# Kernel tuning notes

Measured on AMD Instinct MI355X. Metric: run time of the kernel, lower is better.

The kernel has to match this reference:

```python
import jax, jax.numpy as jnp
import numpy as np

T, B = 2048, 256
NX, NY, NU, ND = 128, 64, 32, 16


def setup_inputs() -> dict:
    key = jax.random.key(0)
    ks = jax.random.split(key, 12)
    # weights scaled to keep the closed-loop recursion numerically stable
    return {
        "Yp": jax.random.normal(ks[0], (T, B, NY), jnp.float32),
        "Up": jax.random.normal(ks[1], (T, B, NU), jnp.float32),
        "Dp": jax.random.normal(ks[2], (T, B, ND), jnp.float32),
        "Wfx": jax.random.normal(ks[3], (NX, NX), jnp.float32) * (0.9 / np.sqrt(NX)),
        "bfx": jax.random.normal(ks[4], (NX,), jnp.float32) * 0.01,
        "Wfu": jax.random.normal(ks[5], (NU, NX), jnp.float32) * (1.0 / np.sqrt(NU)),
        "bfu": jax.random.normal(ks[6], (NX,), jnp.float32) * 0.01,
        "Wfd": jax.random.normal(ks[7], (ND, NX), jnp.float32) * (1.0 / np.sqrt(ND)),
        "bfd": jax.random.normal(ks[8], (NX,), jnp.float32) * 0.01,
        "Wfy": jax.random.normal(ks[9], (NX, NY), jnp.float32) * (1.0 / np.sqrt(NX)),
        "bfy": jax.random.normal(ks[10], (NY,), jnp.float32) * 0.01,
        # constant (non-trainable) filter buffers, matching the torch module
        "Q": jnp.eye(NX, dtype=jnp.float32),
        "R": jnp.eye(NY, dtype=jnp.float32),
        "P0": jnp.eye(NX, dtype=jnp.float32),
        "L0": jnp.zeros((NX, NY), jnp.float32),
        "x0": jnp.zeros((1, NX), jnp.float32),
    }


def reference(Yp, Up, Dp, Wfx, bfx, Wfu, bfu, Wfd, bfd, Wfy, bfy, Q, R, P0, L0, x0):
    nx = Wfx.shape[0]
    Bsz = Yp.shape[1]
    eye = jnp.eye(nx, dtype=Yp.dtype)
    # x0 is zeros(1, nx); broadcast to batch so scan carry has fixed shape
    x_init = jnp.broadcast_to(x0, (Bsz, nx))

    def step(carry, inp):
        x, P, L = carry
        ym, u, d = inp  # [B,ny], [B,nu], [B,nd]
        # prediction (slim linear: x @ W + b)
        x = x @ Wfx + bfx + u @ Wfu + bfu + d @ Wfd + bfd
        y = x @ Wfy + bfy
        P = Wfx @ (P @ Wfx.T) + Q
        # correction with previous gain L (as in the torch code)
        x = x + (ym - y) @ L.T
        S = R + Wfy.T @ (P @ Wfy)              # [ny,ny]
        L = (P @ Wfy) @ jnp.linalg.inv(S)      # [nx,ny]
        P = eye - L @ (Wfy.T @ P)              # faithful to source (I - L H P)
        return (x, P, L), None

    (x, P, L), _ = jax.lax.scan(step, (x_init, P0, L0), (Yp, Up, Dp))
    return x  # 'x0' output of the estimator
```

## Files before the change

kernel.cpp:

```cpp
#include <hip/hip_runtime.h>

#define T_STEPS 2048
#define BATCH   256
#define NXX     128
#define NYY     64
#define NUU     32
#define NDD     16

#define CCH     64
#define NCH     (T_STEPS / CCH)

#define SWZ(i, j) (((i) << 6) + ((j) ^ ((i) & 31)))

__device__ __forceinline__ float4 ld4swz(const float* s, int row, int cg) {
  return *(const float4*)(s + (row << 6) + (cg ^ (row & 28)));
}
__device__ __forceinline__ void st4swz(float* s, int row, int cg, const float4& v) {
  *(float4*)(s + (row << 6) + (cg ^ (row & 28))) = v;
}

__global__ __launch_bounds__(256, 1)
void lkf_gains(const float* __restrict__ F, const float* __restrict__ W,
               const float* __restrict__ Q, const float* __restrict__ R,
               const float* __restrict__ P0, float* __restrict__ Linf,
               float* __restrict__ LinfT, float* __restrict__ CWq,
               float* __restrict__ tmpA, float* __restrict__ tmpB)
{
  __shared__ __align__(16) float sG[NXX * NYY];
  __shared__ __align__(16) float sS[NYY * NYY];
  __shared__ __align__(16) float sM[NYY * NYY];
  __shared__ __align__(16) float sW[NXX * NYY];
  float* sCol = sM;
  float* sRed = sM;
  const int tid = threadIdx.x;

  for (int idx = tid; idx < NXX * NYY; idx += 256)
    sW[SWZ(idx >> 6, idx & 63)] = W[idx];
  for (int idx = tid; idx < NXX * NYY; idx += 256) {
    const int k = idx >> 6, j = idx & 63;
    float acc = 0.f;
    for (int i = 0; i < NXX; ++i) acc += F[i * NXX + k] * W[i * NYY + j];
    tmpA[idx] = acc;
  }
  __syncthreads();
  for (int idx = tid; idx < NXX * NYY; idx += 256) {
    const int i = idx >> 6, j = idx & 63;
    float acc = 0.f;
    for (int k = 0; k < NXX; ++k) acc += F[i * NXX + k] * tmpA[k * NYY + j];
    for (int k = 0; k < NXX; ++k) acc += Q[i * NXX + k] * W[k * NYY + j];
    CWq[idx] = acc;
  }
  for (int idx = tid; idx < NXX * NXX; idx += 256) {
    const int i = idx >> 7, j = idx & 127;
    float acc = 0.f;
    for (int k = 0; k < NXX; ++k) acc += P0[i * NXX + k] * F[j * NXX + k];
    tmpB[idx] = acc;
  }
  __syncthreads();
  for (int idx = tid; idx < NXX * NXX; idx += 256) {
    const int i = idx >> 7, j = idx & 127;
    float acc = Q[idx];
    for (int k = 0; k < NXX; ++k) acc += F[i * NXX + k] * tmpB[k * NXX + j];
    tmpA[idx] = acc;
  }
  __syncthreads();
  for (int idx = tid; idx < NXX * NYY; idx += 256) {
    const int i = idx >> 6, j = idx & 63;
    float acc = 0.f;
    for (int k = 0; k < NXX; ++k) acc += tmpA[i * NXX + k] * W[k * NYY + j];
    sG[SWZ(i, j)] = acc;
  }
  __syncthreads();
  for (int idx = tid; idx < NXX * NXX; idx += 256)
    tmpB[idx] = F[(idx & 127) * NXX + (idx >> 7)];
  const float* Ft = tmpB;

  const int i16 = (tid >> 4) * 4;
  const int j16 = (tid & 15) * 4;
  const int i32 = (tid >> 3) * 4;
  const int j32 = (tid & 7) * 8;

  float cwq[4][8], rreg[4][4];
#pragma unroll
  for (int a = 0; a < 4; ++a)
#pragma unroll
    for (int b = 0; b < 8; ++b)
      cwq[a][b] = CWq[(i32 + a) * NYY + j32 + b];
#pragma unroll
  for (int a = 0; a < 4; ++a)
#pragma unroll
    for (int b = 0; b < 4; ++b)
      rreg[a][b] = R[(i16 + a) * NYY + j16 + b];

  float prevG[4][8], diff[4][8];
#pragma unroll
  for (int a = 0; a < 4; ++a)
#pragma unroll
    for (int b = 0; b < 8; ++b) { prevG[a][b] = 1e30f; diff[a][b] = 0.f; }
  int   cc = 0;
  bool  fin = false;
  float prevDelta = 1e30f;
  __syncthreads();

  for (int t = 0; t < T_STEPS; ++t) {
    {
      float acc[4][4];
#pragma unroll
      for (int a = 0; a < 4; ++a)
#pragma unroll
        for (int b = 0; b < 4; ++b) acc[a][b] = 0.f;
      for (int kb = 0; kb < NXX; kb += 4) {
#pragma unroll
        for (int kk = 0; kk < 4; ++kk) {
          const int k = kb + kk;
          const float4 wv = ld4swz(sW, k, i16);
          const float4 gv = ld4swz(sG, k, j16);
          const float* wf = (const float*)&wv;
          const float* gf = (const float*)&gv;
#pragma unroll
          for (int a = 0; a < 4; ++a)
#pragma unroll
            for (int b = 0; b < 4; ++b)
              acc[a][b] += wf[a ^ kk] * gf[b ^ kk];
        }
      }
#pragma unroll
      for (int a = 0; a < 4; ++a) {
        float4 w; float* wf = (float*)&w;
#pragma unroll
        for (int b = 0; b < 4; ++b) wf[b ^ a] = rreg[a][b] + acc[a][b];
        st4swz(sS, i16 + a, j16, w);
      }
    }
    __syncthreads();

    for (int kb = 0; kb < NYY; kb += 4) {
#pragma unroll
      for (int kk = 0; kk < 4; ++kk) {
        const int k = kb + kk;
        if (tid < NYY) {
          const int j = tid;
          const float piv  = sS[SWZ(k, k)];
          const float pinv = 1.0f / piv;
          const float cv   = sS[SWZ(j, k)];
          sCol[j] = cv;
          if (j != k) {
            sS[SWZ(k, j)] *= pinv;
            sS[SWZ(j, k)] = 0.f;
          } else {
            sS[SWZ(k, k)] = pinv;
          }
        }
        __syncthreads();
        {
          const float4 rk = ld4swz(sS, k, j16);
          const float4 cf = *(const float4*)(sCol + i16);
          const float* rkf = (const float*)&rk;
          const float* cff = (const float*)&cf;
#pragma unroll
          for (int a = 0; a < 4; ++a) {
            if (i16 + a != k) {
              float4 ri = ld4swz(sS, i16 + a, j16);
              float* rif = (float*)&ri;
              const float f = cff[a];
#pragma unroll
              for (int b = 0; b < 4; ++b)
                rif[b ^ a] -= f * rkf[b ^ kk];
              st4swz(sS, i16 + a, j16, ri);
            }
          }
        }
        __syncthreads();
      }
    }

    if (fin || t == T_STEPS - 1) {
      float acc[4][8];
#pragma unroll
      for (int a = 0; a < 4; ++a)
#pragma unroll
        for (int b = 0; b < 8; ++b) acc[a][b] = 0.f;
      for (int k = 0; k < NYY; ++k) {
        float g4[4], s8[8];
#pragma unroll
        for (int a = 0; a < 4; ++a) g4[a] = sG[SWZ(i32 + a, k)];
#pragma unroll
        for (int b = 0; b < 8; ++b) s8[b] = sS[SWZ(k, j32 + b)];
#pragma unroll
        for (int a = 0; a < 4; ++a)
#pragma unroll
          for (int b = 0; b < 8; ++b) acc[a][b] += g4[a] * s8[b];
      }
#pragma unroll
      for (int a = 0; a < 4; ++a)
#pragma unroll
        for (int b = 0; b < 8; ++b) {
          Linf[(i32 + a) * NYY + j32 + b]  = acc[a][b];
          LinfT[(j32 + b) * NXX + i32 + a] = acc[a][b];
        }
      break;
    }

    {
      float acc[4][8];
#pragma unroll
      for (int a = 0; a < 4; ++a)
#pragma unroll
        for (int b = 0; b < 8; ++b) acc[a][b] = 0.f;
      for (int kb = 0; kb < NXX; kb += 4) {
#pragma unroll
        for (int kk = 0; kk < 4; ++kk) {
          const int k = kb + kk;
          const float4 fv  = *(const float4*)(Ft + k * NXX + i32);
          const float4 gv0 = ld4swz(sG, k, j32);
          const float4 gv1 = ld4swz(sG, k, j32 + 4);
          const float* ff  = (const float*)&fv;
          const float* gf0 = (const float*)&gv0;
          const float* gf1 = (const float*)&gv1;
#pragma unroll
          for (int a = 0; a < 4; ++a)
#pragma unroll
            for (int b = 0; b < 4; ++b) {
              acc[a][b]     += ff[a] * gf0[b ^ kk];
              acc[a][b + 4] += ff[a] * gf1[b ^ kk];
            }
        }
      }
      __syncthreads();
#pragma unroll
      for (int a = 0; a < 4; ++a) {
        float4 w0, w1; float* wf0 = (float*)&w0; float* wf1 = (float*)&w1;
#pragma unroll
        for (int b = 0; b < 4; ++b) {
          wf0[b ^ a] = acc[a][b];
          wf1[b ^ a] = acc[a][b + 4];
        }
        st4swz(sG, i32 + a, j32, w0);
        st4swz(sG, i32 + a, j32 + 4, w1);
      }
    }
    __syncthreads();

    {
      float acc[4][4];
#pragma unroll
      for (int a = 0; a < 4; ++a)
#pragma unroll
        for (int b = 0; b < 4; ++b) acc[a][b] = 0.f;
      for (int kb = 0; kb < NXX; kb += 4) {
#pragma unroll
        for (int kk = 0; kk < 4; ++kk) {
          const int k = kb + kk;
          const float4 hv = ld4swz(sG, k, i16);
          const float4 wv = ld4swz(sW, k, j16);
          const float* hf = (const float*)&hv;
          const float* wf = (const float*)&wv;
#pragma unroll
          for (int a = 0; a < 4; ++a)
#pragma unroll
            for (int b = 0; b < 4; ++b)
              acc[a][b] += hf[a ^ kk] * wf[b ^ kk];
        }
      }
#pragma unroll
      for (int a = 0; a < 4; ++a) {
        float4 w; float* wf = (float*)&w;
#pragma unroll
        for (int b = 0; b < 4; ++b) wf[b ^ a] = acc[a][b];
        st4swz(sM, i16 + a, j16, w);
      }
    }
    __syncthreads();

    {
      float acc[4][4];
#pragma unroll
      for (int a = 0; a < 4; ++a)
#pragma unroll
        for (int b = 0; b < 4; ++b) acc[a][b] = 0.f;
      for (int kb = 0; kb < NYY; kb += 4) {
        float4 sv[4];
#pragma unroll
        for (int a = 0; a < 4; ++a) sv[a] = ld4swz(sS, i16 + a, kb);
#pragma unroll
        for (int kk = 0; kk < 4; ++kk) {
          const float4 mv = ld4swz(sM, kb + kk, j16);
          const float* mf = (const float*)&mv;
#pragma unroll
          for (int a = 0; a < 4; ++a) {
            const float s = ((const float*)&sv[a])[kk ^ a];
#pragma unroll
            for (int b = 0; b < 4; ++b)
              acc[a][b] += s * mf[b ^ kk];
          }
        }
      }
      __syncthreads();
#pragma unroll
      for (int a = 0; a < 4; ++a) {
        float4 w; float* wf = (float*)&w;
#pragma unroll
        for (int b = 0; b < 4; ++b) wf[b ^ a] = acc[a][b];
        st4swz(sS, i16 + a, j16, w);
      }
    }
    __syncthreads();

    float gdelta = 0.f;
    {
      float acc[4][8];
#pragma unroll
      for (int a = 0; a < 4; ++a)
#pragma unroll
        for (int b = 0; b < 8; ++b) acc[a][b] = 0.f;
      for (int kb = 0; kb < NYY; kb += 4) {
        float4 hv[4];
#pragma unroll
        for (int a = 0; a < 4; ++a) hv[a] = ld4swz(sG, i32 + a, kb);
#pragma unroll
        for (int kk = 0; kk < 4; ++kk) {
          const float4 xv0 = ld4swz(sS, kb + kk, j32);
          const float4 xv1 = ld4swz(sS, kb + kk, j32 + 4);
          const float* xf0 = (const float*)&xv0;
          const float* xf1 = (const float*)&xv1;
#pragma unroll
          for (int a = 0; a < 4; ++a) {
            const float h = ((const float*)&hv[a])[kk ^ a];
#pragma unroll
            for (int b = 0; b < 4; ++b) {
              acc[a][b]     += h * xf0[b ^ kk];
              acc[a][b + 4] += h * xf1[b ^ kk];
            }
          }
        }
      }
      __syncthreads();
#pragma unroll
      for (int a = 0; a < 4; ++a) {
        float4 w0, w1; float* wf0 = (float*)&w0; float* wf1 = (float*)&w1;
#pragma unroll
        for (int b = 0; b < 4; ++b) {
          const float g0 = cwq[a][b]     - acc[a][b];
          const float g1 = cwq[a][b + 4] - acc[a][b + 4];
          wf0[b ^ a] = g0;
          wf1[b ^ a] = g1;
          const float d0 = g0 - prevG[a][b];
          const float d1 = g1 - prevG[a][b + 4];
          diff[a][b] = d0; diff[a][b + 4] = d1;
          gdelta = fmaxf(gdelta, fmaxf(fabsf(d0), fabsf(d1)));
          prevG[a][b] = g0; prevG[a][b + 4] = g1;
        }
        st4swz(sG, i32 + a, j32, w0);
        st4swz(sG, i32 + a, j32 + 4, w1);
      }
    }
    __syncthreads();
    sRed[tid] = gdelta;
    __syncthreads();
    if (tid < 64) {
      float m = fmaxf(fmaxf(sRed[tid], sRed[tid + 64]),
                      fmaxf(sRed[tid + 128], sRed[tid + 192]));
#pragma unroll
      for (int off = 32; off >= 1; off >>= 1)
        m = fmaxf(m, __shfl_down(m, off));
      if (tid == 0) sRed[0] = m;
    }
    __syncthreads();
    const float delta = sRed[0];
    const float r     = delta / prevDelta;
    prevDelta = delta;
    cc = (delta < 3e-5f) ? cc + 1 : 0;
    if (cc >= 2) fin = true;
    __syncthreads();

    if (!fin && t >= 40 && ((t - 8) & 31) == 0 && r > 0.5f && r < 0.99f) {
      const float alpha = fminf(r / (1.0f - r), 25.0f);
#pragma unroll
      for (int a = 0; a < 4; ++a)
#pragma unroll
        for (int b = 0; b < 8; ++b) {
          const float g = prevG[a][b] + alpha * diff[a][b];
          sG[SWZ(i32 + a, j32 + b)] = g;
          prevG[a][b] = g;
        }
      __syncthreads();
    }
  }
}

__global__ __launch_bounds__(64, 1)
void lkf_fuse(const float* __restrict__ F, const float* __restrict__ Wfu,
              const float* __restrict__ Wfd, const float* __restrict__ Wy,
              const float* __restrict__ bfx, const float* __restrict__ bfu,
              const float* __restrict__ bfd, const float* __restrict__ bfy,
              const float* __restrict__ Linf, float* __restrict__ Az,
              float* __restrict__ Buz, float* __restrict__ Bdz,
              float* __restrict__ cz)
{
  __shared__ float srow[NXX];
  __shared__ float fw[NYY];
  const int w = blockIdx.x, tid = threadIdx.x;

  for (int k = tid; k < NXX; k += 64) {
    float v;
    if (w < 128)      v = F[w * NXX + k];
    else if (w < 160) v = Wfu[(w - 128) * NXX + k];
    else if (w < 176) v = Wfd[(w - 160) * NXX + k];
    else              v = bfx[k] + bfu[k] + bfd[k];
    srow[k] = v;
  }
  __syncthreads();
  {
    const int m = tid;
    float acc = (w == 176) ? bfy[m] : 0.f;
    for (int k = 0; k < NXX; ++k) acc += srow[k] * Wy[k * NYY + m];
    fw[m] = acc;
  }
  __syncthreads();
  for (int j = tid; j < NXX; j += 64) {
    float s = 0.f;
    for (int m = 0; m < NYY; ++m) s += fw[m] * Linf[j * NYY + m];
    const float val = srow[j] - s;
    if (w < 128)      Az[w * NXX + j] = val;
    else if (w < 160) Buz[(w - 128) * NXX + j] = val;
    else if (w < 176) Bdz[(w - 160) * NXX + j] = val;
    else              cz[j] = val;
  }
}

__global__ __launch_bounds__(256, 1)
void mat_sq(const float* __restrict__ in, float* __restrict__ out)
{
  const int gid = blockIdx.x * 256 + threadIdx.x;
  const int i = gid >> 7, j = gid & 127;
  float acc = 0.f;
  for (int k = 0; k < NXX; ++k) acc += in[i * NXX + k] * in[k * NXX + j];
  out[gid] = acc;
}

__global__ __launch_bounds__(256, 2)
void lkf_chunk(const float* __restrict__ Yp, const float* __restrict__ Up,
               const float* __restrict__ Dp, const float* __restrict__ Az,
               const float* __restrict__ Buz, const float* __restrict__ Bdz,
               const float* __restrict__ cz, const float* __restrict__ LinfT,
               float* __restrict__ V)
{
  __shared__ __align__(16) float xs[2][NXX];
  __shared__ __align__(16) float ymb[2][NYY];
  __shared__ __align__(16) float ub[2][NUU];
  __shared__ __align__(16) float db[2][NDD];
  __shared__ float ps[NXX];

  const int tid = threadIdx.x;
  const int b   = blockIdx.x;
  const int c   = blockIdx.y;
  const int j   = tid & 127;
  const int h   = tid >> 7;

  float a[64], l[32], bu[16], bd[8];
#pragma unroll
  for (int k = 0; k < 64; ++k) a[k] = Az[(h * 64 + k) * NXX + j];
#pragma unroll
  for (int m = 0; m < 32; ++m) l[m] = LinfT[(h * 32 + m) * NXX + j];
#pragma unroll
  for (int k = 0; k < 16; ++k) bu[k] = Buz[(h * 16 + k) * NXX + j];
#pragma unroll
  for (int k = 0; k < 8; ++k)  bd[k] = Bdz[(h * 8 + k) * NXX + j];
  const float cj = (h == 0) ? cz[j] : 0.f;

  const int t0 = c * CCH;
  if (tid < 128) xs[0][tid] = 0.f;
  {
    const size_t tb = (size_t)t0 * BATCH + b;
    if (tid < 64)       ymb[0][tid]     = Yp[tb * NYY + tid];
    else if (tid < 96)  ub[0][tid - 64] = Up[tb * NUU + (tid - 64)];
    else if (tid < 112) db[0][tid - 96] = Dp[tb * NDD + (tid - 96)];
  }
  __syncthreads();

  for (int s = 0; s < CCH; ++s) {
    const int p = s & 1;

    float pf = 0.f;
    if (s < CCH - 1) {
      const size_t tb = (size_t)(t0 + s + 1) * BATCH + b;
      if (tid < 64)       pf = Yp[tb * NYY + tid];
      else if (tid < 96)  pf = Up[tb * NUU + (tid - 64)];
      else if (tid < 112) pf = Dp[tb * NDD + (tid - 96)];
    }

    float acc0 = cj, acc1 = 0.f, acc2 = 0.f, acc3 = 0.f;
    {
      const float4* x4 = (const float4*)(xs[p] + h * 64);
#pragma unroll
      for (int k4 = 0; k4 < 16; ++k4) {
        const float4 xv = x4[k4];
        acc0 += xv.x * a[4 * k4 + 0];
        acc1 += xv.y * a[4 * k4 + 1];
        acc2 += xv.z * a[4 * k4 + 2];
        acc3 += xv.w * a[4 * k4 + 3];
      }
      const float4* y4 = (const float4*)(ymb[p] + h * 32);
#pragma unroll
      for (int m4 = 0; m4 < 8; ++m4) {
        const float4 yv = y4[m4];
        acc0 += yv.x * l[4 * m4 + 0];
        acc1 += yv.y * l[4 * m4 + 1];
        acc2 += yv.z * l[4 * m4 + 2];
        acc3 += yv.w * l[4 * m4 + 3];
      }
      const float4* u4 = (const float4*)(ub[p] + h * 16);
#pragma unroll
      for (int k4 = 0; k4 < 4; ++k4) {
        const float4 uv = u4[k4];
        acc0 += uv.x * bu[4 * k4 + 0];
        acc1 += uv.y * bu[4 * k4 + 1];
        acc2 += uv.z * bu[4 * k4 + 2];
        acc3 += uv.w * bu[4 * k4 + 3];
      }
      const float4* d4 = (const float4*)(db[p] + h * 8);
#pragma unroll
      for (int k4 = 0; k4 < 2; ++k4) {
        const float4 dv = d4[k4];
        acc0 += dv.x * bd[4 * k4 + 0];
        acc1 += dv.y * bd[4 * k4 + 1];
        acc2 += dv.z * bd[4 * k4 + 2];
        acc3 += dv.w * bd[4 * k4 + 3];
      }
    }
    const float part = (acc0 + acc1) + (acc2 + acc3);
    if (h == 1) ps[j] = part;
    __syncthreads();
    if (h == 0) xs[1 - p][j] = part + ps[j];
    if (s < CCH - 1) {
      if (tid < 64)       ymb[1 - p][tid]     = pf;
      else if (tid < 96)  ub[1 - p][tid - 64] = pf;
      else if (tid < 112) db[1 - p][tid - 96] = pf;
    }
    __syncthreads();
  }

  if (tid < 128)
    V[((size_t)b * NCH + c) * NXX + tid] = xs[0][tid];
}

__global__ __launch_bounds__(128, 1)
void lkf_comb(const float* __restrict__ A64, const float* __restrict__ V,
              const float* __restrict__ x0, float* __restrict__ out)
{
  __shared__ __align__(16) float xs[2][NXX];
  const int tid = threadIdx.x;
  const int b   = blockIdx.x;
  float a[NXX];
#pragma unroll
  for (int k = 0; k < NXX; ++k) a[k] = A64[k * NXX + tid];
  xs[0][tid] = x0[tid];
  __syncthreads();
  for (int c = 0; c < NCH; ++c) {
    const int p = c & 1;
    float acc0 = V[((size_t)b * NCH + c) * NXX + tid];
    float acc1 = 0.f, acc2 = 0.f, acc3 = 0.f;
    const float4* x4 = (const float4*)xs[p];
#pragma unroll
    for (int k4 = 0; k4 < NXX / 4; ++k4) {
      const float4 xv = x4[k4];
      acc0 += xv.x * a[4 * k4 + 0];
      acc1 += xv.y * a[4 * k4 + 1];
      acc2 += xv.z * a[4 * k4 + 2];
      acc3 += xv.w * a[4 * k4 + 3];
    }
    xs[1 - p][tid] = (acc0 + acc1) + (acc2 + acc3);
    __syncthreads();
  }
  out[(size_t)b * NXX + tid] = xs[0][tid];
}

__global__ __launch_bounds__(128, 1)
void lkf_state(const float* __restrict__ Yp, const float* __restrict__ Up,
               const float* __restrict__ Dp, const float* __restrict__ Az,
               const float* __restrict__ Buz, const float* __restrict__ Bdz,
               const float* __restrict__ cz, const float* __restrict__ LinfT,
               const float* __restrict__ x0, float* __restrict__ out)
{
  __shared__ __align__(16) float xs[2][NXX];
  __shared__ __align__(16) float ymb[2][NYY];
  __shared__ __align__(16) float ub[2][NUU];
  __shared__ __align__(16) float db[2][NDD];

  const int tid = threadIdx.x;
  const int b   = blockIdx.x;
  const int j   = tid;

  float a[NXX], l[NYY], bu[NUU], bd[NDD];
#pragma unroll
  for (int k = 0; k < NXX; ++k) a[k] = Az[k * NXX + j];
#pragma unroll
  for (int m = 0; m < NYY; ++m) l[m] = LinfT[m * NXX + j];
#pragma unroll
  for (int k = 0; k < NUU; ++k) bu[k] = Buz[k * NXX + j];
#pragma unroll
  for (int k = 0; k < NDD; ++k) bd[k] = Bdz[k * NXX + j];
  const float cj = cz[j];

  xs[0][tid] = x0[tid];
  if (tid < 64)       ymb[0][tid]     = Yp[(size_t)b * NYY + tid];
  else if (tid < 96)  ub[0][tid - 64] = Up[(size_t)b * NUU + (tid - 64)];
  else if (tid < 112) db[0][tid - 96] = Dp[(size_t)b * NDD + (tid - 96)];
  __syncthreads();

  for (int t = 0; t < T_STEPS; ++t) {
    const int p = t & 1;
    float pf = 0.f;
    if (t < T_STEPS - 1) {
      const size_t tb = (size_t)(t + 1) * BATCH + b;
      if (tid < 64)       pf = Yp[tb * NYY + tid];
      else if (tid < 96)  pf = Up[tb * NUU + (tid - 64)];
      else if (tid < 112) pf = Dp[tb * NDD + (tid - 96)];
    }

    float acc0 = cj, acc1 = 0.f, acc2 = 0.f, acc3 = 0.f;
    {
      const float4* x4 = (const float4*)xs[p];
#pragma unroll
      for (int k4 = 0; k4 < NXX / 4; ++k4) {
        const float4 xv = x4[k4];
        acc0 += xv.x * a[4 * k4 + 0];
        acc1 += xv.y * a[4 * k4 + 1];
        acc2 += xv.z * a[4 * k4 + 2];
        acc3 += xv.w * a[4 * k4 + 3];
      }
      const float4* y4 = (const float4*)ymb[p];
#pragma unroll
      for (int m4 = 0; m4 < NYY / 4; ++m4) {
        const float4 yv = y4[m4];
        acc0 += yv.x * l[4 * m4 + 0];
        acc1 += yv.y * l[4 * m4 + 1];
        acc2 += yv.z * l[4 * m4 + 2];
        acc3 += yv.w * l[4 * m4 + 3];
      }
      const float4* u4 = (const float4*)ub[p];
#pragma unroll
      for (int k4 = 0; k4 < NUU / 4; ++k4) {
        const float4 uv = u4[k4];
        acc0 += uv.x * bu[4 * k4 + 0];
        acc1 += uv.y * bu[4 * k4 + 1];
        acc2 += uv.z * bu[4 * k4 + 2];
        acc3 += uv.w * bu[4 * k4 + 3];
      }
      const float4* d4 = (const float4*)db[p];
#pragma unroll
      for (int k4 = 0; k4 < NDD / 4; ++k4) {
        const float4 dv = d4[k4];
        acc0 += dv.x * bd[4 * k4 + 0];
        acc1 += dv.y * bd[4 * k4 + 1];
        acc2 += dv.z * bd[4 * k4 + 2];
        acc3 += dv.w * bd[4 * k4 + 3];
      }
    }
    xs[1 - p][j] = (acc0 + acc1) + (acc2 + acc3);

    if (t < T_STEPS - 1) {
      if (tid < 64)       ymb[1 - p][tid]     = pf;
      else if (tid < 96)  ub[1 - p][tid - 64] = pf;
      else if (tid < 112) db[1 - p][tid - 96] = pf;
    }
    __syncthreads();
  }

  out[(size_t)b * NXX + j] = xs[0][j];
}

extern "C" void kernel_launch(void* const* d_in, const int* in_sizes, int n_in,
                              void* d_out, int out_size, void* d_ws,
                              size_t ws_size, hipStream_t stream) {
  const float* Yp  = (const float*)d_in[0];
  const float* Up  = (const float*)d_in[1];
  const float* Dp  = (const float*)d_in[2];
  const float* Wfx = (const float*)d_in[3];
  const float* bfx = (const float*)d_in[4];
  const float* Wfu = (const float*)d_in[5];
  const float* bfu = (const float*)d_in[6];
  const float* Wfd = (const float*)d_in[7];
  const float* bfd = (const float*)d_in[8];
  const float* Wfy = (const float*)d_in[9];
  const float* bfy = (const float*)d_in[10];
  const float* Q   = (const float*)d_in[11];
  const float* R   = (const float*)d_in[12];
  const float* P0  = (const float*)d_in[13];
  const float* x0  = (const float*)d_in[15];

  float* ws    = (float*)d_ws;
  float* Linf  = ws;
  float* LinfT = Linf  + NXX * NYY;
  float* CWq   = LinfT + NYY * NXX;
  float* tmpA  = CWq   + NXX * NYY;
  float* tmpB  = tmpA  + NXX * NXX;
  float* Az    = tmpB  + NXX * NXX;
  float* Buz   = Az    + NXX * NXX;
  float* Bdz   = Buz   + NUU * NXX;
  float* cz    = Bdz   + NDD * NXX;
  float* pA    = cz    + NXX;
  float* pB    = pA    + NXX * NXX;
  float* V     = pB    + NXX * NXX;

  const size_t needBytes =
      ((size_t)(V - ws) + (size_t)BATCH * NCH * NXX) * sizeof(float);

  lkf_gains<<<dim3(1), dim3(256), 0, stream>>>(Wfx, Wfy, Q, R, P0, Linf, LinfT,
                                               CWq, tmpA, tmpB);
  lkf_fuse<<<dim3(177), dim3(64), 0, stream>>>(Wfx, Wfu, Wfd, Wfy, bfx, bfu,
                                               bfd, bfy, Linf, Az, Buz, Bdz,
                                               cz);

  if (ws_size >= needBytes) {
    mat_sq<<<dim3(64), dim3(256), 0, stream>>>(Az, pA);
    mat_sq<<<dim3(64), dim3(256), 0, stream>>>(pA, pB);
    mat_sq<<<dim3(64), dim3(256), 0, stream>>>(pB, pA);
    mat_sq<<<dim3(64), dim3(256), 0, stream>>>(pA, pB);
    mat_sq<<<dim3(64), dim3(256), 0, stream>>>(pB, pA);
    mat_sq<<<dim3(64), dim3(256), 0, stream>>>(pA, pB);
    lkf_chunk<<<dim3(BATCH, NCH), dim3(256), 0, stream>>>(
        Yp, Up, Dp, Az, Buz, Bdz, cz, LinfT, V);
    lkf_comb<<<dim3(BATCH), dim3(128), 0, stream>>>(pB, V, x0, (float*)d_out);
  } else {
    lkf_state<<<dim3(BATCH), dim3(128), 0, stream>>>(
        Yp, Up, Dp, Az, Buz, Bdz, cz, LinfT, x0, (float*)d_out);
  }
}
```

Measured before the change: 2.826 ms.

## Block Gauss-Jordan inversion in gains kernel; preload chunk inputs into LDS

The 64x64 Gauss-Jordan inversion in lkf_gains now eliminates a 4x4 pivot block per step held in registers, then applies a block rank-4 update. This cuts the barrier count from two per pivot to two per four pivots. Separately, lkf_chunk loads all 64 timesteps of Y/U/D for its chunk into shared memory with float4 loads up front, replacing the per-step scalar global prefetch. The costs are extra per-thread register work, about 28KB of LDS per block, and block pivoting without row exchange, which is numerically fine for the SPD S.

```diff
diff --git a/kernel.cpp b/kernel.cpp
--- a/kernel.cpp
+++ b/kernel.cpp
@@ -30,7 +30,6 @@
   __shared__ __align__(16) float sS[NYY * NYY];
   __shared__ __align__(16) float sM[NYY * NYY];
   __shared__ __align__(16) float sW[NXX * NYY];
-  float* sCol = sM;
   float* sRed = sM;
   const int tid = threadIdx.x;
 
@@ -135,43 +134,82 @@
     __syncthreads();
 
     for (int kb = 0; kb < NYY; kb += 4) {
-#pragma unroll
-      for (int kk = 0; kk < 4; ++kk) {
-        const int k = kb + kk;
-        if (tid < NYY) {
-          const int j = tid;
-          const float piv  = sS[SWZ(k, k)];
-          const float pinv = 1.0f / piv;
-          const float cv   = sS[SWZ(j, k)];
-          sCol[j] = cv;
-          if (j != k) {
-            sS[SWZ(k, j)] *= pinv;
-            sS[SWZ(j, k)] = 0.f;
-          } else {
-            sS[SWZ(k, k)] = pinv;
+      float d[4][4], r[4][4], cb[4][4], o[4][4];
+#pragma unroll
+      for (int a = 0; a < 4; ++a) {
+        const float4 Dv = ld4swz(sS, kb + a, kb);
+        const float4 Rv = ld4swz(sS, kb + a, j16);
+        const float4 Cv = ld4swz(sS, i16 + a, kb);
+        const float4 Ov = ld4swz(sS, i16 + a, j16);
+        const float* Df = (const float*)&Dv;
+        const float* Rf = (const float*)&Rv;
+        const float* Cf = (const float*)&Cv;
+        const float* Of = (const float*)&Ov;
+#pragma unroll
+        for (int b = 0; b < 4; ++b) {
+          d[a][b]  = Df[b ^ a];
+          r[a][b]  = Rf[b ^ a];
+          cb[a][b] = Cf[b ^ a];
+          o[a][b]  = Of[b ^ a];
+        }
+      }
+#pragma unroll
+      for (int k = 0; k < 4; ++k) {
+        const float p = 1.0f / d[k][k];
+#pragma unroll
+        for (int j = 0; j < 4; ++j) if (j != k) d[k][j] *= p;
+        float cv[4];
+#pragma unroll
+        for (int i = 0; i < 4; ++i) cv[i] = d[i][k];
+        d[k][k] = p;
+#pragma unroll
+        for (int i = 0; i < 4; ++i) if (i != k) {
+#pragma unroll
+          for (int j = 0; j < 4; ++j) if (j != k) d[i][j] -= cv[i] * d[k][j];
+          d[i][k] = -cv[i] * p;
+        }
+      }
+      float tT[4][4], uU[4][4], vV[4][4];
+#pragma unroll
+      for (int a = 0; a < 4; ++a)
+#pragma unroll
+        for (int b = 0; b < 4; ++b) {
+          float s1 = 0.f, s2 = 0.f;
+#pragma unroll
+          for (int k = 0; k < 4; ++k) {
+            s1 += d[a][k] * r[k][b];
+            s2 += cb[a][k] * d[k][b];
           }
-        }
-        __syncthreads();
-        {
-          const float4 rk = ld4swz(sS, k, j16);
-          const float4 cf = *(const float4*)(sCol + i16);
-          const float* rkf = (const float*)&rk;
-          const float* cff = (const float*)&cf;
-#pragma unroll
-          for (int a = 0; a < 4; ++a) {
-            if (i16 + a != k) {
-              float4 ri = ld4swz(sS, i16 + a, j16);
-              float* rif = (float*)&ri;
-              const float f = cff[a];
-#pragma unroll
-              for (int b = 0; b < 4; ++b)
-                rif[b ^ a] -= f * rkf[b ^ kk];
-              st4swz(sS, i16 + a, j16, ri);
-            }
+          tT[a][b] = s1; uU[a][b] = s2;
+        }
+#pragma unroll
+      for (int a = 0; a < 4; ++a)
+#pragma unroll
+        for (int b = 0; b < 4; ++b) {
+          float s = 0.f;
+#pragma unroll
+          for (int k = 0; k < 4; ++k) s += cb[a][k] * tT[k][b];
+          vV[a][b] = s;
+        }
+      __syncthreads();
+      {
+        const bool rowB = (i16 == kb), colB = (j16 == kb);
+#pragma unroll
+        for (int a = 0; a < 4; ++a) {
+          float4 w; float* wf = (float*)&w;
+#pragma unroll
+          for (int b = 0; b < 4; ++b) {
+            float val;
+            if (rowB && colB)  val = d[a][b];
+            else if (rowB)     val = tT[a][b];
+            else if (colB)     val = -uU[a][b];
+            else               val = o[a][b] - vV[a][b];
+            wf[b ^ a] = val;
           }
-        }
-        __syncthreads();
-      }
+          st4swz(sS, i16 + a, j16, w);
+        }
+      }
+      __syncthreads();
     }
 
     if (fin || t == T_STEPS - 1) {
@@ -445,10 +483,8 @@
                const float* __restrict__ cz, const float* __restrict__ LinfT,
                float* __restrict__ V)
 {
+  __shared__ __align__(16) float4 inL[1792];
   __shared__ __align__(16) float xs[2][NXX];
-  __shared__ __align__(16) float ymb[2][NYY];
-  __shared__ __align__(16) float ub[2][NUU];
-  __shared__ __align__(16) float db[2][NDD];
   __shared__ float ps[NXX];
 
   const int tid = threadIdx.x;
@@ -469,26 +505,32 @@
   const float cj = (h == 0) ? cz[j] : 0.f;
 
   const int t0 = c * CCH;
+  {
+    const float4* Y4 = (const float4*)Yp;
+    const float4* U4 = (const float4*)Up;
+    const float4* D4 = (const float4*)Dp;
+#pragma unroll
+    for (int q = 0; q < 7; ++q) {
+      const int idx = q * 256 + tid;
+      float4 v;
+      if (q < 4) {
+        const int s = idx >> 4, f = idx & 15;
+        v = Y4[((size_t)(t0 + s) * BATCH + b) * (NYY / 4) + f];
+      } else if (q < 6) {
+        const int rel = idx - 1024, s = rel >> 3, f = rel & 7;
+        v = U4[((size_t)(t0 + s) * BATCH + b) * (NUU / 4) + f];
+      } else {
+        const int rel = idx - 1536, s = rel >> 2, f = rel & 3;
+        v = D4[((size_t)(t0 + s) * BATCH + b) * (NDD / 4) + f];
+      }
+      inL[idx] = v;
+    }
+  }
   if (tid < 128) xs[0][tid] = 0.f;
-  {
-    const size_t tb = (size_t)t0 * BATCH + b;
-    if (tid < 64)       ymb[0][tid]     = Yp[tb * NYY + tid];
-    else if (tid < 96)  ub[0][tid - 64] = Up[tb * NUU + (tid - 64)];
-    else if (tid < 112) db[0][tid - 96] = Dp[tb * NDD + (tid - 96)];
-  }
   __syncthreads();
 
   for (int s = 0; s < CCH; ++s) {
     const int p = s & 1;
-
-    float pf = 0.f;
-    if (s < CCH - 1) {
-      const size_t tb = (size_t)(t0 + s + 1) * BATCH + b;
-      if (tid < 64)       pf = Yp[tb * NYY + tid];
-      else if (tid < 96)  pf = Up[tb * NUU + (tid - 64)];
-      else if (tid < 112) pf = Dp[tb * NDD + (tid - 96)];
-    }
-
     float acc0 = cj, acc1 = 0.f, acc2 = 0.f, acc3 = 0.f;
     {
       const float4* x4 = (const float4*)(xs[p] + h * 64);
@@ -500,7 +542,7 @@
         acc2 += xv.z * a[4 * k4 + 2];
         acc3 += xv.w * a[4 * k4 + 3];
       }
-      const float4* y4 = (const float4*)(ymb[p] + h * 32);
+      const float4* y4 = inL + s * 16 + h * 8;
 #pragma unroll
       for (int m4 = 0; m4 < 8; ++m4) {
         const float4 yv = y4[m4];
@@ -509,7 +551,7 @@
         acc2 += yv.z * l[4 * m4 + 2];
         acc3 += yv.w * l[4 * m4 + 3];
       }
-      const float4* u4 = (const float4*)(ub[p] + h * 16);
+      const float4* u4 = inL + 1024 + s * 8 + h * 4;
 #pragma unroll
       for (int k4 = 0; k4 < 4; ++k4) {
         const float4 uv = u4[k4];
@@ -518,7 +560,7 @@
         acc2 += uv.z * bu[4 * k4 + 2];
         acc3 += uv.w * bu[4 * k4 + 3];
       }
-      const float4* d4 = (const float4*)(db[p] + h * 8);
+      const float4* d4 = inL + 1536 + s * 4 + h * 2;
 #pragma unroll
       for (int k4 = 0; k4 < 2; ++k4) {
         const float4 dv = d4[k4];
@@ -532,11 +574,6 @@
     if (h == 1) ps[j] = part;
     __syncthreads();
     if (h == 0) xs[1 - p][j] = part + ps[j];
-    if (s < CCH - 1) {
-      if (tid < 64)       ymb[1 - p][tid]     = pf;
-      else if (tid < 96)  ub[1 - p][tid - 64] = pf;
-      else if (tid < 112) db[1 - p][tid - 96] = pf;
-    }
     __syncthreads();
   }
 
```

Measured after the change: 2.582 ms. -8.6%, faster.
